# Optimization experiments

Hardware: AMD Instinct MI355X
Metric: run time of the kernel (lower is better)

## Reference

```python
import jax, jax.numpy as jnp
import numpy as np

N_NODES = 100000
EMB = 256
N_MP_EDGES = 1600000
N_SUP_EDGES = 200000


def _sage_conv(x, src, dst, W_l, b_l, W_r, n_nodes):
    # PyG SAGEConv (aggr='mean', project=False):
    #   out = lin_l(mean_{j->i} x_j) + lin_r(x_i)
    # message flows edge_index[0] (src) -> edge_index[1] (dst)
    summed = jax.ops.segment_sum(x[src], dst, num_segments=n_nodes)          # [N, d]
    cnt = jax.ops.segment_sum(jnp.ones((src.shape[0],), x.dtype), dst,
                              num_segments=n_nodes)                          # [N]
    mean = summed / jnp.maximum(cnt, 1.0)[:, None]
    return mean @ W_l.T + b_l + x @ W_r.T


def setup_inputs() -> dict:
    key = jax.random.key(0)
    ks = jax.random.split(key, 12)
    scale = 1.0 / np.sqrt(EMB)
    inp = {
        "node_embeddings": jax.random.normal(ks[0], (N_NODES, EMB), jnp.float32),
        "message_passing_edge_index": jax.random.randint(ks[1], (2, N_MP_EDGES), 0, N_NODES, jnp.int64),
        "supervision_edge_index": jax.random.randint(ks[2], (2, N_SUP_EDGES), 0, N_NODES, jnp.int64),
    }
    for i in range(3):
        inp[f"W_l{i+1}"] = jax.random.normal(ks[3 + 3 * i], (EMB, EMB), jnp.float32) * scale
        inp[f"b_l{i+1}"] = jnp.zeros((EMB,), jnp.float32)
        inp[f"W_r{i+1}"] = jax.random.normal(ks[4 + 3 * i], (EMB, EMB), jnp.float32) * scale
    return inp


def reference(node_embeddings, message_passing_edge_index, supervision_edge_index,
              W_l1, b_l1, W_r1, W_l2, b_l2, W_r2, W_l3, b_l3, W_r3):
    src = message_passing_edge_index[0]
    dst = message_passing_edge_index[1]
    n = node_embeddings.shape[0]

    x = _sage_conv(node_embeddings, src, dst, W_l1, b_l1, W_r1, n)
    x = jax.nn.relu(x)
    x = _sage_conv(x, src, dst, W_l2, b_l2, W_r2, n)
    x = jax.nn.relu(x)
    x = _sage_conv(x, src, dst, W_l3, b_l3, W_r3, n)

    s = supervision_edge_index[0]
    d = supervision_edge_index[1]
    scores = jnp.sum(x[s] * x[d], axis=1)  # [n_sup_edges]
    return scores
```

## Files before the change

kernel.cpp:

```cpp
#include <hip/hip_runtime.h>
#include <hip/hip_bf16.h>

#define N_NODES 100000
#define EMB 256
#define N_MP 1600000
#define N_SUP 200000

typedef __attribute__((ext_vector_type(4))) float f32x4;
typedef __attribute__((ext_vector_type(2))) float f32x2;
typedef __attribute__((ext_vector_type(8))) short s16x8;
typedef unsigned char uchar;

__device__ __forceinline__ int clampi(int v, int lo, int hi) {
    return v < lo ? lo : (v > hi ? hi : v);
}
__device__ __forceinline__ ushort f2bf(float f) {
    unsigned u = __float_as_uint(f);
    u += 0x7fffu + ((u >> 16) & 1u);
    return (ushort)(u >> 16);
}
__device__ __forceinline__ float bf2f(ushort h) {
    return __uint_as_float(((unsigned)h) << 16);
}
template <bool HI>
__device__ __forceinline__ f32x2 fp8_to_f32x2(unsigned w) {
    return __builtin_amdgcn_cvt_pk_f32_fp8(w, HI);
}
__device__ __forceinline__ unsigned f32x2_to_fp8(float a, float b) {
    return (unsigned)__builtin_amdgcn_cvt_pk_fp8_f32(a, b, 0, false) & 0xffffu;
}

#define GLOAD_LDS16(gsrc, ldst)                                                   \
    __builtin_amdgcn_global_load_lds(                                             \
        (const __attribute__((address_space(1))) void*)(gsrc),                    \
        (__attribute__((address_space(3))) void*)(ldst), 16, 0, 0)


__global__ void f2b8_kernel(const float* __restrict__ in, ushort* __restrict__ outb,
                            uchar* __restrict__ out8, int n8) {
    int i = blockIdx.x * 256 + threadIdx.x;
    if (i >= n8) return;
    const float4* p = (const float4*)(in + (size_t)i * 8);
    float4 a = p[0], b = p[1];
    ushort4 lo = make_ushort4(f2bf(a.x), f2bf(a.y), f2bf(a.z), f2bf(a.w));
    ushort4 hi = make_ushort4(f2bf(b.x), f2bf(b.y), f2bf(b.z), f2bf(b.w));
    ushort4* q = (ushort4*)(outb + (size_t)i * 8);
    q[0] = lo; q[1] = hi;
    uint2 f8;
    f8.x = f32x2_to_fp8(a.x, a.y) | (f32x2_to_fp8(a.z, a.w) << 16);
    f8.y = f32x2_to_fp8(b.x, b.y) | (f32x2_to_fp8(b.z, b.w) << 16);
    *(uint2*)(out8 + (size_t)i * 8) = f8;
}

struct W6 { const float* p[6]; };
__global__ void wcvt_kernel(W6 ws, ushort* __restrict__ outbase) {
    int m = blockIdx.x >> 5;
    int idx = (blockIdx.x & 31) * 256 + threadIdx.x;
    const float4* p = (const float4*)(ws.p[m] + (size_t)idx * 8);
    float4 a = p[0], b = p[1];
    ushort4 lo = make_ushort4(f2bf(a.x), f2bf(a.y), f2bf(a.z), f2bf(a.w));
    ushort4 hi = make_ushort4(f2bf(b.x), f2bf(b.y), f2bf(b.z), f2bf(b.w));
    ushort4* q = (ushort4*)(outbase + (size_t)m * EMB * EMB + (size_t)idx * 8);
    q[0] = lo; q[1] = hi;
}


#define BSH 9
#define NBUCK ((N_NODES + 511) / 512)
#define EPB_A 4096
#define SCAP 16384

__global__ void binit_kernel(int* __restrict__ gbfill) {
    int t = threadIdx.x;
    if (t < NBUCK) gbfill[t] = t * SCAP;
}

__global__ __launch_bounds__(1024) void bin_kernel(
    const int* __restrict__ src, const int* __restrict__ dst, int n,
    int* __restrict__ gbfill, unsigned* __restrict__ packed) {
    __shared__ int cnt[256];
    __shared__ int base[256];
    int tid = threadIdx.x;
    if (tid < 256) cnt[tid] = 0;
    __syncthreads();
    int e0 = blockIdx.x * EPB_A + tid;
    int bk[4], rank[4], sv[4];
    bool valid[4];
#pragma unroll
    for (int k = 0; k < 4; ++k) {
        int e = e0 + k * 1024;
        valid[k] = e < n;
        if (valid[k]) {
            int d = clampi(dst[e], 0, N_NODES - 1);
            sv[k] = clampi(src[e], 0, N_NODES - 1);
            bk[k] = d >> BSH;
            int dl = d & 511;
            sv[k] |= (dl << 20);
            rank[k] = atomicAdd(&cnt[bk[k]], 1);
        }
    }
    __syncthreads();
    if (tid < 256) {
        int c = cnt[tid];
        base[tid] = c > 0 ? atomicAdd(&gbfill[tid], c) : 0;
    }
    __syncthreads();
#pragma unroll
    for (int k = 0; k < 4; ++k) {
        if (valid[k]) {
            int pos = base[bk[k]] + rank[k];
            if (pos < (bk[k] + 1) * SCAP) packed[pos] = (unsigned)sv[k];
        }
    }
}

__global__ void bscan_kernel(const int* __restrict__ gbfill, int* __restrict__ bbase,
                             int* __restrict__ rp) {
    __shared__ int c[256];
    int t = threadIdx.x;
    c[t] = (t < NBUCK) ? (gbfill[t] - t * SCAP) : 0;
    __syncthreads();
    if (t == 0) {
        int run = 0;
        for (int i = 0; i < NBUCK; ++i) { int v = c[i]; c[i] = run; run += v; }
        rp[N_NODES] = run;
    }
    __syncthreads();
    if (t < NBUCK) bbase[t] = c[t];
}

__global__ __launch_bounds__(1024) void debin_kernel(
    const unsigned* __restrict__ packed, const int* __restrict__ gbfill,
    const int* __restrict__ bbase, int* __restrict__ srt, int* __restrict__ rp) {
    __shared__ int cnt[512];
    __shared__ int loc[512];
    __shared__ int wsum[8];
    int b = blockIdx.x;
    int tid = threadIdx.x;
    int lane = tid & 63, wv = tid >> 6;
    int node0 = b << BSH;
    int nn = N_NODES - node0; if (nn > 512) nn = 512;
    if (tid < 512) cnt[tid] = 0;
    __syncthreads();
    int pbase = b * SCAP;
    int bcnt = gbfill[b] - pbase;
    if (bcnt > SCAP) bcnt = SCAP;
    for (int e = tid; e < bcnt; e += 1024)
        atomicAdd(&cnt[packed[pbase + e] >> 20], 1);
    __syncthreads();
    int v = (tid < 512) ? cnt[tid] : 0;
    int t = v;
#pragma unroll
    for (int off = 1; off < 64; off <<= 1) {
        int u = __shfl_up(t, off, 64);
        if (lane >= off) t += u;
    }
    if (tid < 512 && lane == 63) wsum[wv] = t;
    __syncthreads();
    if (tid < 512) {
        int woff = 0;
        for (int i = 0; i < wv; ++i) woff += wsum[i];
        loc[tid] = woff + t - v;
        if (tid < nn) rp[node0 + tid] = bbase[b] + loc[tid];
    }
    __syncthreads();
    if (tid < 512) cnt[tid] = 0;
    __syncthreads();
    int sb = bbase[b];
    for (int e = tid; e < bcnt; e += 1024) {
        unsigned p = packed[pbase + e];
        int dl = p >> 20;
        int rank = atomicAdd(&cnt[dl], 1);
        srt[sb + loc[dl] + rank] = (int)(p & 0xFFFFFu);
    }
}


__global__ void agg_kernel(const uchar* __restrict__ x8, const int* __restrict__ rp,
                           const int* __restrict__ srt, ushort* __restrict__ outm) {
    int w = threadIdx.x >> 6;
    int lane = threadIdx.x & 63;
    int qw = lane >> 4;
    int sl = lane & 15;
    int node = blockIdx.x * 4 + w;
    if (node >= N_NODES) return;
    int beg = rp[node], end = rp[node + 1];
    int deg = end - beg;
    float acc[16];
#pragma unroll
    for (int i = 0; i < 16; ++i) acc[i] = 0.f;

    for (int bse = 0; bse < deg; bse += 64) {
        int rem = deg - bse;
        int cnt = rem < 64 ? rem : 64;
        int myidx = (lane < cnt) ? srt[beg + bse + lane] : 0;
        for (int j = 0; j < cnt; j += 4) {
            int e = j + qw;
            int s = __shfl(myidx, e < cnt ? e : 0, 64);
            if (e < cnt) {
                uint4 v = *(const uint4*)&x8[(unsigned)s * EMB + sl * 16];
                f32x2 p;
                p = fp8_to_f32x2<false>(v.x); acc[0] += p.x; acc[1] += p.y;
                p = fp8_to_f32x2<true >(v.x); acc[2] += p.x; acc[3] += p.y;
                p = fp8_to_f32x2<false>(v.y); acc[4] += p.x; acc[5] += p.y;
                p = fp8_to_f32x2<true >(v.y); acc[6] += p.x; acc[7] += p.y;
                p = fp8_to_f32x2<false>(v.z); acc[8] += p.x; acc[9] += p.y;
                p = fp8_to_f32x2<true >(v.z); acc[10] += p.x; acc[11] += p.y;
                p = fp8_to_f32x2<false>(v.w); acc[12] += p.x; acc[13] += p.y;
                p = fp8_to_f32x2<true >(v.w); acc[14] += p.x; acc[15] += p.y;
            }
        }
    }
#pragma unroll
    for (int i = 0; i < 16; ++i) acc[i] += __shfl_xor(acc[i], 32, 64);
#pragma unroll
    for (int i = 0; i < 16; ++i) acc[i] += __shfl_xor(acc[i], 16, 64);
    float inv = 1.0f / fmaxf((float)deg, 1.0f);
    if (qw == 0) {
        s16x8 o0, o1;
#pragma unroll
        for (int i = 0; i < 8; ++i) o0[i] = (short)f2bf(acc[i] * inv);
#pragma unroll
        for (int i = 0; i < 8; ++i) o1[i] = (short)f2bf(acc[8 + i] * inv);
        *(s16x8*)&outm[(size_t)node * EMB + sl * 16] = o0;
        *(s16x8*)&outm[(size_t)node * EMB + sl * 16 + 8] = o1;
    }
}


#define BM 128
#define BN 256
#define BKG 32
#define NSTEPS 16
#define ABSZ (BM * BKG)
#define BUFSZ (BM * BKG + BN * BKG)

__global__ __launch_bounds__(512) void gemm_kernel(
    const ushort* __restrict__ Am, const ushort* __restrict__ Ax,
    const ushort* __restrict__ Wl, const ushort* __restrict__ Wr,
    const float* __restrict__ bias, ushort* __restrict__ out,
    uchar* __restrict__ out8, int M, int do_relu) {
    __shared__ ushort smem[3 * BUFSZ];
    const int tid = threadIdx.x;
    const int lane = tid & 63;
    const int w = tid >> 6;
    const int m0 = blockIdx.x * BM;
    const int wr = w >> 2;
    const int wc = w & 3;

    f32x4 acc[4][4];
#pragma unroll
    for (int i = 0; i < 4; ++i)
#pragma unroll
        for (int j = 0; j < 4; ++j) acc[i][j] = (f32x4){0.f, 0.f, 0.f, 0.f};

    int ca = tid;
    int ra = ca >> 2;
    int cca = (ca & 3) ^ (ra & 3);
    int arow = m0 + ra; if (arow > M - 1) arow = M - 1;
    size_t srcA = (size_t)arow * EMB + cca * 8;
    int ldsoA = ca * 8;
    int cb0 = tid, cb1 = tid + 512;
    int rb0 = cb0 >> 2, rb1 = cb1 >> 2;
    size_t srcB0 = (size_t)rb0 * EMB + ((cb0 & 3) ^ (rb0 & 3)) * 8;
    size_t srcB1 = (size_t)rb1 * EMB + ((cb1 & 3) ^ (rb1 & 3)) * 8;
    int ldsoB0 = cb0 * 8, ldsoB1 = cb1 * 8;

    int raf[4], rbf[4];
#pragma unroll
    for (int mf = 0; mf < 4; ++mf) {
        int r = wr * 64 + mf * 16 + (lane & 15);
        raf[mf] = r * BKG + (((lane >> 4) ^ (r & 3)) * 8);
    }
#pragma unroll
    for (int nf = 0; nf < 4; ++nf) {
        int r = wc * 64 + nf * 16 + (lane & 15);
        rbf[nf] = r * BKG + (((lane >> 4) ^ (r & 3)) * 8);
    }

    GLOAD_LDS16(Am + srcA, smem + ldsoA);
    GLOAD_LDS16(Wl + srcB0, smem + ABSZ + ldsoB0);
    GLOAD_LDS16(Wl + srcB1, smem + ABSZ + ldsoB1);
    GLOAD_LDS16(Am + srcA + BKG, smem + BUFSZ + ldsoA);
    GLOAD_LDS16(Wl + srcB0 + BKG, smem + BUFSZ + ABSZ + ldsoB0);
    GLOAD_LDS16(Wl + srcB1 + BKG, smem + BUFSZ + ABSZ + ldsoB1);

    for (int s = 0; s < NSTEPS; ++s) {
        if (s < NSTEPS - 1) {
            asm volatile("s_waitcnt vmcnt(3)" ::: "memory");
        } else {
            asm volatile("s_waitcnt vmcnt(0)" ::: "memory");
        }
        __builtin_amdgcn_s_barrier();
        __builtin_amdgcn_sched_barrier(0);
        int nx = s + 2;
        if (nx < NSTEPS) {
            const ushort* A = (nx >= 8) ? Ax : Am;
            const ushort* W = (nx >= 8) ? Wr : Wl;
            int k0 = (nx & 7) * BKG;
            ushort* d = smem + (nx % 3) * BUFSZ;
            GLOAD_LDS16(A + srcA + k0, d + ldsoA);
            GLOAD_LDS16(W + srcB0 + k0, d + ABSZ + ldsoB0);
            GLOAD_LDS16(W + srcB1 + k0, d + ABSZ + ldsoB1);
        }
        const ushort* As = smem + (s % 3) * BUFSZ;
        const ushort* Bs = As + ABSZ;
        s16x8 af[4], bg[4];
#pragma unroll
        for (int mf = 0; mf < 4; ++mf) af[mf] = *(const s16x8*)&As[raf[mf]];
#pragma unroll
        for (int nf = 0; nf < 4; ++nf) bg[nf] = *(const s16x8*)&Bs[rbf[nf]];
#pragma unroll
        for (int mf = 0; mf < 4; ++mf)
#pragma unroll
            for (int nf = 0; nf < 4; ++nf)
                acc[mf][nf] = __builtin_amdgcn_mfma_f32_16x16x32_bf16(
                    af[mf], bg[nf], acc[mf][nf], 0, 0, 0);
    }
    __syncthreads();

    ushort* Cs = smem;
#pragma unroll
    for (int p = 0; p < 2; ++p) {
        if (wr == p) {
#pragma unroll
            for (int nf = 0; nf < 4; ++nf) {
                int col = wc * 64 + nf * 16 + (lane & 15);
                float bv = bias[col];
#pragma unroll
                for (int mf = 0; mf < 4; ++mf) {
                    int rl = mf * 16 + ((lane >> 4) << 2);
#pragma unroll
                    for (int q = 0; q < 4; ++q) {
                        float v = acc[mf][nf][q] + bv;
                        if (do_relu) v = fmaxf(v, 0.f);
                        Cs[(rl + q) * BN + col] = f2bf(v);
                    }
                }
            }
        }
        __syncthreads();
#pragma unroll
        for (int i = 0; i < 4; ++i) {
            int idx = i * 512 + tid;
            int row = m0 + p * 64 + (idx >> 5);
            if (row < M) {
                uint4 v = ((const uint4*)Cs)[idx];
                *(uint4*)&out[(size_t)row * EMB + (idx & 31) * 8] = v;
                if (out8) {
                    const ushort* pu = (const ushort*)&v;
                    unsigned lo = f32x2_to_fp8(bf2f(pu[0]), bf2f(pu[1])) |
                                  (f32x2_to_fp8(bf2f(pu[2]), bf2f(pu[3])) << 16);
                    unsigned hi = f32x2_to_fp8(bf2f(pu[4]), bf2f(pu[5])) |
                                  (f32x2_to_fp8(bf2f(pu[6]), bf2f(pu[7])) << 16);
                    *(uint2*)&out8[(size_t)row * EMB + (idx & 31) * 8] =
                        make_uint2(lo, hi);
                }
            }
        }
        __syncthreads();
    }
}


__global__ void score_kernel(const ushort* __restrict__ x, const int* __restrict__ sup,
                             float* __restrict__ out) {
    int w = threadIdx.x >> 6;
    int lane = threadIdx.x & 63;
    int half = lane >> 5;
    int sl = lane & 31;
    int e = blockIdx.x * 4 + w;
    if (e >= N_SUP) return;
    int s = clampi(sup[e], 0, N_NODES - 1);
    int d = clampi(sup[N_SUP + e], 0, N_NODES - 1);
    int row = half ? d : s;
    uint4 raw = *(const uint4*)&x[(unsigned)row * EMB + sl * 8];
    uint4 pr;
    pr.x = __shfl_xor(raw.x, 32, 64);
    pr.y = __shfl_xor(raw.y, 32, 64);
    pr.z = __shfl_xor(raw.z, 32, 64);
    pr.w = __shfl_xor(raw.w, 32, 64);
    float t = 0.f;
    unsigned a[4] = {raw.x, raw.y, raw.z, raw.w};
    unsigned b[4] = {pr.x, pr.y, pr.z, pr.w};
#pragma unroll
    for (int i = 0; i < 4; ++i) {
        t += bf2f((ushort)(a[i] & 0xffff)) * bf2f((ushort)(b[i] & 0xffff));
        t += bf2f((ushort)(a[i] >> 16)) * bf2f((ushort)(b[i] >> 16));
    }
#pragma unroll
    for (int off = 16; off > 0; off >>= 1) t += __shfl_xor(t, off, 64);
    if (lane == 0) out[e] = t;
}


extern "C" void kernel_launch(void* const* d_in, const int* in_sizes, int n_in,
                              void* d_out, int out_size, void* d_ws, size_t ws_size,
                              hipStream_t stream) {
    const float* x0  = (const float*)d_in[0];
    const int*   mp  = (const int*)d_in[1];
    const int*   sup = (const int*)d_in[2];
    W6 wsrc;
    wsrc.p[0] = (const float*)d_in[3];
    wsrc.p[1] = (const float*)d_in[5];
    wsrc.p[2] = (const float*)d_in[6];
    wsrc.p[3] = (const float*)d_in[8];
    wsrc.p[4] = (const float*)d_in[9];
    wsrc.p[5] = (const float*)d_in[11];
    const float* bl1 = (const float*)d_in[4];
    const float* bl2 = (const float*)d_in[7];
    const float* bl3 = (const float*)d_in[10];
    float* scores = (float*)d_out;

    const int* mp_src = mp;
    const int* mp_dst = mp + N_MP;

    char* base = (char*)d_ws;
    size_t off = 0;
    auto alloc = [&](size_t bytes) {
        void* p = base + off;
        off = (off + bytes + 255) & ~(size_t)255;
        return p;
    };
    int* rp     = (int*)alloc((N_NODES + 1) * sizeof(int));
    int* gbfill = (int*)alloc(256 * sizeof(int));
    int* bbase  = (int*)alloc(256 * sizeof(int));
    int* srt    = (int*)alloc(N_MP * sizeof(int));
    unsigned* packed = (unsigned*)alloc((size_t)NBUCK * SCAP * sizeof(unsigned));
    ushort* x0b  = (ushort*)alloc((size_t)N_NODES * EMB * sizeof(ushort));
    ushort* bufA = (ushort*)alloc((size_t)N_NODES * EMB * sizeof(ushort));
    ushort* bufB = (ushort*)alloc((size_t)N_NODES * EMB * sizeof(ushort));
    ushort* bufC = (ushort*)alloc((size_t)N_NODES * EMB * sizeof(ushort));
    uchar*  x0f8 = (uchar*)alloc((size_t)N_NODES * EMB);
    uchar*  a8   = (uchar*)alloc((size_t)N_NODES * EMB);
    ushort* Wb   = (ushort*)alloc((size_t)6 * EMB * EMB * sizeof(ushort));
    (void)ws_size; (void)n_in; (void)in_sizes; (void)out_size;

    f2b8_kernel<<<(N_NODES * EMB / 8 + 255) / 256, 256, 0, stream>>>(
        x0, x0b, x0f8, N_NODES * EMB / 8);
    wcvt_kernel<<<192, 256, 0, stream>>>(wsrc, Wb);

    binit_kernel<<<1, 256, 0, stream>>>(gbfill);
    bin_kernel<<<(N_MP + EPB_A - 1) / EPB_A, 1024, 0, stream>>>(
        mp_src, mp_dst, N_MP, gbfill, packed);
    bscan_kernel<<<1, 256, 0, stream>>>(gbfill, bbase, rp);
    debin_kernel<<<NBUCK, 1024, 0, stream>>>(packed, gbfill, bbase, srt, rp);

    dim3 gemm_grid((N_NODES + BM - 1) / BM, 1);
    int agg_blocks = (N_NODES + 3) / 4;

    ushort* Wl1 = Wb + 0 * EMB * EMB; ushort* Wr1 = Wb + 1 * EMB * EMB;
    ushort* Wl2 = Wb + 2 * EMB * EMB; ushort* Wr2 = Wb + 3 * EMB * EMB;
    ushort* Wl3 = Wb + 4 * EMB * EMB; ushort* Wr3 = Wb + 5 * EMB * EMB;

    agg_kernel<<<agg_blocks, 256, 0, stream>>>(x0f8, rp, srt, bufC);
    gemm_kernel<<<gemm_grid, 512, 0, stream>>>(bufC, x0b, Wl1, Wr1, bl1, bufA, a8, N_NODES, 1);

    agg_kernel<<<agg_blocks, 256, 0, stream>>>(a8, rp, srt, bufC);
    gemm_kernel<<<gemm_grid, 512, 0, stream>>>(bufC, bufA, Wl2, Wr2, bl2, bufB, a8, N_NODES, 1);

    agg_kernel<<<agg_blocks, 256, 0, stream>>>(a8, rp, srt, bufC);
    gemm_kernel<<<gemm_grid, 512, 0, stream>>>(bufC, bufB, Wl3, Wr3, bl3, bufA,
                                               (uchar*)nullptr, N_NODES, 0);

    score_kernel<<<(N_SUP + 3) / 4, 256, 0, stream>>>(bufA, sup, scores);
}
```

Before: 434.7 us.

## Store aggregated means in fp8 and run the lin_l GEMM half with fp8 MFMA

```diff
diff --git a/kernel.cpp b/kernel.cpp
--- a/kernel.cpp
+++ b/kernel.cpp
@@ -53,15 +53,21 @@
 }
 
 struct W6 { const float* p[6]; };
-__global__ void wcvt_kernel(W6 ws, ushort* __restrict__ outbase) {
+__global__ void wcvt_kernel(W6 ws, ushort* __restrict__ outb, uchar* __restrict__ out8) {
     int m = blockIdx.x >> 5;
     int idx = (blockIdx.x & 31) * 256 + threadIdx.x;
     const float4* p = (const float4*)(ws.p[m] + (size_t)idx * 8);
     float4 a = p[0], b = p[1];
     ushort4 lo = make_ushort4(f2bf(a.x), f2bf(a.y), f2bf(a.z), f2bf(a.w));
     ushort4 hi = make_ushort4(f2bf(b.x), f2bf(b.y), f2bf(b.z), f2bf(b.w));
-    ushort4* q = (ushort4*)(outbase + (size_t)m * EMB * EMB + (size_t)idx * 8);
+    ushort4* q = (ushort4*)(outb + (size_t)m * EMB * EMB + (size_t)idx * 8);
     q[0] = lo; q[1] = hi;
+    if (!(m & 1)) {
+        uint2 f8;
+        f8.x = f32x2_to_fp8(a.x, a.y) | (f32x2_to_fp8(a.z, a.w) << 16);
+        f8.y = f32x2_to_fp8(b.x, b.y) | (f32x2_to_fp8(b.z, b.w) << 16);
+        *(uint2*)(out8 + (size_t)(m >> 1) * EMB * EMB + (size_t)idx * 8) = f8;
+    }
 }
 
 
@@ -177,7 +183,7 @@
 
 
 __global__ void agg_kernel(const uchar* __restrict__ x8, const int* __restrict__ rp,
-                           const int* __restrict__ srt, ushort* __restrict__ outm) {
+                           const int* __restrict__ srt, uchar* __restrict__ outm8) {
     int w = threadIdx.x >> 6;
     int lane = threadIdx.x & 63;
     int qw = lane >> 4;
@@ -217,27 +223,29 @@
     for (int i = 0; i < 16; ++i) acc[i] += __shfl_xor(acc[i], 16, 64);
     float inv = 1.0f / fmaxf((float)deg, 1.0f);
     if (qw == 0) {
-        s16x8 o0, o1;
-#pragma unroll
-        for (int i = 0; i < 8; ++i) o0[i] = (short)f2bf(acc[i] * inv);
-#pragma unroll
-        for (int i = 0; i < 8; ++i) o1[i] = (short)f2bf(acc[8 + i] * inv);
-        *(s16x8*)&outm[(size_t)node * EMB + sl * 16] = o0;
-        *(s16x8*)&outm[(size_t)node * EMB + sl * 16 + 8] = o1;
+        uint4 o;
+        o.x = f32x2_to_fp8(acc[0] * inv, acc[1] * inv) |
+              (f32x2_to_fp8(acc[2] * inv, acc[3] * inv) << 16);
+        o.y = f32x2_to_fp8(acc[4] * inv, acc[5] * inv) |
+              (f32x2_to_fp8(acc[6] * inv, acc[7] * inv) << 16);
+        o.z = f32x2_to_fp8(acc[8] * inv, acc[9] * inv) |
+              (f32x2_to_fp8(acc[10] * inv, acc[11] * inv) << 16);
+        o.w = f32x2_to_fp8(acc[12] * inv, acc[13] * inv) |
+              (f32x2_to_fp8(acc[14] * inv, acc[15] * inv) << 16);
+        *(uint4*)&outm8[(size_t)node * EMB + sl * 16] = o;
     }
 }
 
 
 #define BM 128
 #define BN 256
-#define BKG 32
-#define NSTEPS 16
-#define ABSZ (BM * BKG)
-#define BUFSZ (BM * BKG + BN * BKG)
+#define NSTEPS 12
+#define BUFSZ 12288
+#define AREG 8192
 
 __global__ __launch_bounds__(512) void gemm_kernel(
-    const ushort* __restrict__ Am, const ushort* __restrict__ Ax,
-    const ushort* __restrict__ Wl, const ushort* __restrict__ Wr,
+    const uchar* __restrict__ Am8, const ushort* __restrict__ Ax,
+    const uchar* __restrict__ Wl8, const ushort* __restrict__ Wr,
     const float* __restrict__ bias, ushort* __restrict__ out,
     uchar* __restrict__ out8, int M, int do_relu) {
     __shared__ ushort smem[3 * BUFSZ];
@@ -247,6 +255,7 @@
     const int m0 = blockIdx.x * BM;
     const int wr = w >> 2;
     const int wc = w & 3;
+    const int g = lane >> 4;
 
     f32x4 acc[4][4];
 #pragma unroll
@@ -254,36 +263,54 @@
 #pragma unroll
         for (int j = 0; j < 4; ++j) acc[i][j] = (f32x4){0.f, 0.f, 0.f, 0.f};
 
-    int ca = tid;
-    int ra = ca >> 2;
-    int cca = (ca & 3) ^ (ra & 3);
-    int arow = m0 + ra; if (arow > M - 1) arow = M - 1;
-    size_t srcA = (size_t)arow * EMB + cca * 8;
-    int ldsoA = ca * 8;
-    int cb0 = tid, cb1 = tid + 512;
-    int rb0 = cb0 >> 2, rb1 = cb1 >> 2;
-    size_t srcB0 = (size_t)rb0 * EMB + ((cb0 & 3) ^ (rb0 & 3)) * 8;
-    size_t srcB1 = (size_t)rb1 * EMB + ((cb1 & 3) ^ (rb1 & 3)) * 8;
-    int ldsoB0 = cb0 * 8, ldsoB1 = cb1 * 8;
-
-    int raf[4], rbf[4];
+    int cA = tid;
+    int rA = cA >> 2, qA = (cA & 3) ^ (rA & 3);
+    int arow = m0 + rA; if (arow > M - 1) arow = M - 1;
+    int cB0 = tid, cB1 = tid + 512;
+    int rB0 = cB0 >> 2, qB0 = (cB0 & 3) ^ (rB0 & 3);
+    int rB1 = cB1 >> 2, qB1 = (cB1 & 3) ^ (rB1 & 3);
+    size_t srcA8 = (size_t)arow * 256 + qA * 16;
+    size_t srcB08 = (size_t)rB0 * 256 + qB0 * 16;
+    size_t srcB18 = (size_t)rB1 * 256 + qB1 * 16;
+    size_t srcAb = (size_t)arow * EMB + qA * 8;
+    size_t srcB0b = (size_t)rB0 * EMB + qB0 * 8;
+    size_t srcB1b = (size_t)rB1 * EMB + qB1 * 8;
+    int ldsoA = cA * 16;
+    int ldsoB0 = AREG + cB0 * 16;
+    int ldsoB1 = AREG + cB1 * 16;
+
+    int raf8[4][2], rbf8[4][2], rafb[4], rbfb[4];
 #pragma unroll
     for (int mf = 0; mf < 4; ++mf) {
         int r = wr * 64 + mf * 16 + (lane & 15);
-        raf[mf] = r * BKG + (((lane >> 4) ^ (r & 3)) * 8);
+        rafb[mf] = r * 64 + (((g) ^ (r & 3)) << 4);
+#pragma unroll
+        for (int ks = 0; ks < 2; ++ks) {
+            int hi = ks * 2 + (g >> 1);
+            raf8[mf][ks] = r * 64 + ((hi ^ (r & 3)) << 4) + ((g & 1) * 8);
+        }
     }
 #pragma unroll
     for (int nf = 0; nf < 4; ++nf) {
         int r = wc * 64 + nf * 16 + (lane & 15);
-        rbf[nf] = r * BKG + (((lane >> 4) ^ (r & 3)) * 8);
-    }
-
-    GLOAD_LDS16(Am + srcA, smem + ldsoA);
-    GLOAD_LDS16(Wl + srcB0, smem + ABSZ + ldsoB0);
-    GLOAD_LDS16(Wl + srcB1, smem + ABSZ + ldsoB1);
-    GLOAD_LDS16(Am + srcA + BKG, smem + BUFSZ + ldsoA);
-    GLOAD_LDS16(Wl + srcB0 + BKG, smem + BUFSZ + ABSZ + ldsoB0);
-    GLOAD_LDS16(Wl + srcB1 + BKG, smem + BUFSZ + ABSZ + ldsoB1);
+        rbfb[nf] = r * 64 + (((g) ^ (r & 3)) << 4);
+#pragma unroll
+        for (int ks = 0; ks < 2; ++ks) {
+            int hi = ks * 2 + (g >> 1);
+            rbf8[nf][ks] = r * 64 + ((hi ^ (r & 3)) << 4) + ((g & 1) * 8);
+        }
+    }
+
+    {
+        uchar* d0 = (uchar*)smem;
+        uchar* d1 = (uchar*)smem + BUFSZ * 2;
+        GLOAD_LDS16(Am8 + srcA8 + 0, d0 + ldsoA);
+        GLOAD_LDS16(Wl8 + srcB08 + 0, d0 + ldsoB0);
+        GLOAD_LDS16(Wl8 + srcB18 + 0, d0 + ldsoB1);
+        GLOAD_LDS16(Am8 + srcA8 + 64, d1 + ldsoA);
+        GLOAD_LDS16(Wl8 + srcB08 + 64, d1 + ldsoB0);
+        GLOAD_LDS16(Wl8 + srcB18 + 64, d1 + ldsoB1);
+    }
 
     for (int s = 0; s < NSTEPS; ++s) {
         if (s < NSTEPS - 1) {
@@ -295,27 +322,55 @@
         __builtin_amdgcn_sched_barrier(0);
         int nx = s + 2;
         if (nx < NSTEPS) {
-            const ushort* A = (nx >= 8) ? Ax : Am;
-            const ushort* W = (nx >= 8) ? Wr : Wl;
-            int k0 = (nx & 7) * BKG;
-            ushort* d = smem + (nx % 3) * BUFSZ;
-            GLOAD_LDS16(A + srcA + k0, d + ldsoA);
-            GLOAD_LDS16(W + srcB0 + k0, d + ABSZ + ldsoB0);
-            GLOAD_LDS16(W + srcB1 + k0, d + ABSZ + ldsoB1);
-        }
-        const ushort* As = smem + (s % 3) * BUFSZ;
-        const ushort* Bs = As + ABSZ;
-        s16x8 af[4], bg[4];
-#pragma unroll
-        for (int mf = 0; mf < 4; ++mf) af[mf] = *(const s16x8*)&As[raf[mf]];
-#pragma unroll
-        for (int nf = 0; nf < 4; ++nf) bg[nf] = *(const s16x8*)&Bs[rbf[nf]];
-#pragma unroll
-        for (int mf = 0; mf < 4; ++mf)
-#pragma unroll
-            for (int nf = 0; nf < 4; ++nf)
-                acc[mf][nf] = __builtin_amdgcn_mfma_f32_16x16x32_bf16(
-                    af[mf], bg[nf], acc[mf][nf], 0, 0, 0);
+            uchar* d = (uchar*)smem + (nx % 3) * BUFSZ * 2;
+            if (nx < 4) {
+                int k0 = nx * 64;
+                GLOAD_LDS16(Am8 + srcA8 + k0, d + ldsoA);
+                GLOAD_LDS16(Wl8 + srcB08 + k0, d + ldsoB0);
+                GLOAD_LDS16(Wl8 + srcB18 + k0, d + ldsoB1);
+            } else {
+                int k0 = (nx - 4) * 32;
+                GLOAD_LDS16(Ax + srcAb + k0, d + ldsoA);
+                GLOAD_LDS16(Wr + srcB0b + k0, d + ldsoB0);
+                GLOAD_LDS16(Wr + srcB1b + k0, d + ldsoB1);
+            }
+        }
+        const char* Asb = (const char*)smem + (s % 3) * BUFSZ * 2;
+        const char* Bsb = Asb + AREG;
+        if (s < 4) {
+            long af[4][2], bg[4][2];
+#pragma unroll
+            for (int mf = 0; mf < 4; ++mf) {
+                af[mf][0] = *(const long*)(Asb + raf8[mf][0]);
+                af[mf][1] = *(const long*)(Asb + raf8[mf][1]);
+            }
+#pragma unroll
+            for (int nf = 0; nf < 4; ++nf) {
+                bg[nf][0] = *(const long*)(Bsb + rbf8[nf][0]);
+                bg[nf][1] = *(const long*)(Bsb + rbf8[nf][1]);
+            }
+#pragma unroll
+            for (int mf = 0; mf < 4; ++mf)
+#pragma unroll
+                for (int nf = 0; nf < 4; ++nf) {
+                    acc[mf][nf] = __builtin_amdgcn_mfma_f32_16x16x32_fp8_fp8(
+                        af[mf][0], bg[nf][0], acc[mf][nf], 0, 0, 0);
+                    acc[mf][nf] = __builtin_amdgcn_mfma_f32_16x16x32_fp8_fp8(
+                        af[mf][1], bg[nf][1], acc[mf][nf], 0, 0, 0);
+                }
+        } else {
+            s16x8 af[4], bg[4];
+#pragma unroll
+            for (int mf = 0; mf < 4; ++mf) af[mf] = *(const s16x8*)(Asb + rafb[mf]);
+#pragma unroll
+            for (int nf = 0; nf < 4; ++nf) bg[nf] = *(const s16x8*)(Bsb + rbfb[nf]);
+#pragma unroll
+            for (int mf = 0; mf < 4; ++mf)
+#pragma unroll
+                for (int nf = 0; nf < 4; ++nf)
+                    acc[mf][nf] = __builtin_amdgcn_mfma_f32_16x16x32_bf16(
+                        af[mf], bg[nf], acc[mf][nf], 0, 0, 0);
+        }
     }
     __syncthreads();
 
@@ -430,15 +485,16 @@
     ushort* x0b  = (ushort*)alloc((size_t)N_NODES * EMB * sizeof(ushort));
     ushort* bufA = (ushort*)alloc((size_t)N_NODES * EMB * sizeof(ushort));
     ushort* bufB = (ushort*)alloc((size_t)N_NODES * EMB * sizeof(ushort));
-    ushort* bufC = (ushort*)alloc((size_t)N_NODES * EMB * sizeof(ushort));
+    uchar*  bufC8 = (uchar*)alloc((size_t)N_NODES * EMB);
     uchar*  x0f8 = (uchar*)alloc((size_t)N_NODES * EMB);
     uchar*  a8   = (uchar*)alloc((size_t)N_NODES * EMB);
     ushort* Wb   = (ushort*)alloc((size_t)6 * EMB * EMB * sizeof(ushort));
+    uchar*  W8   = (uchar*)alloc((size_t)3 * EMB * EMB);
     (void)ws_size; (void)n_in; (void)in_sizes; (void)out_size;
 
     f2b8_kernel<<<(N_NODES * EMB / 8 + 255) / 256, 256, 0, stream>>>(
         x0, x0b, x0f8, N_NODES * EMB / 8);
-    wcvt_kernel<<<192, 256, 0, stream>>>(wsrc, Wb);
+    wcvt_kernel<<<192, 256, 0, stream>>>(wsrc, Wb, W8);
 
     binit_kernel<<<1, 256, 0, stream>>>(gbfill);
     bin_kernel<<<(N_MP + EPB_A - 1) / EPB_A, 1024, 0, stream>>>(
@@ -449,18 +505,21 @@
     dim3 gemm_grid((N_NODES + BM - 1) / BM, 1);
     int agg_blocks = (N_NODES + 3) / 4;
 
-    ushort* Wl1 = Wb + 0 * EMB * EMB; ushort* Wr1 = Wb + 1 * EMB * EMB;
-    ushort* Wl2 = Wb + 2 * EMB * EMB; ushort* Wr2 = Wb + 3 * EMB * EMB;
-    ushort* Wl3 = Wb + 4 * EMB * EMB; ushort* Wr3 = Wb + 5 * EMB * EMB;
-
-    agg_kernel<<<agg_blocks, 256, 0, stream>>>(x0f8, rp, srt, bufC);
-    gemm_kernel<<<gemm_grid, 512, 0, stream>>>(bufC, x0b, Wl1, Wr1, bl1, bufA, a8, N_NODES, 1);
-
-    agg_kernel<<<agg_blocks, 256, 0, stream>>>(a8, rp, srt, bufC);
-    gemm_kernel<<<gemm_grid, 512, 0, stream>>>(bufC, bufA, Wl2, Wr2, bl2, bufB, a8, N_NODES, 1);
-
-    agg_kernel<<<agg_blocks, 256, 0, stream>>>(a8, rp, srt, bufC);
-    gemm_kernel<<<gemm_grid, 512, 0, stream>>>(bufC, bufB, Wl3, Wr3, bl3, bufA,
+    ushort* Wr1 = Wb + 1 * EMB * EMB;
+    ushort* Wr2 = Wb + 3 * EMB * EMB;
+    ushort* Wr3 = Wb + 5 * EMB * EMB;
+    uchar* Wl1_8 = W8 + 0 * EMB * EMB;
+    uchar* Wl2_8 = W8 + 1 * EMB * EMB;
+    uchar* Wl3_8 = W8 + 2 * EMB * EMB;
+
+    agg_kernel<<<agg_blocks, 256, 0, stream>>>(x0f8, rp, srt, bufC8);
+    gemm_kernel<<<gemm_grid, 512, 0, stream>>>(bufC8, x0b, Wl1_8, Wr1, bl1, bufA, a8, N_NODES, 1);
+
+    agg_kernel<<<agg_blocks, 256, 0, stream>>>(a8, rp, srt, bufC8);
+    gemm_kernel<<<gemm_grid, 512, 0, stream>>>(bufC8, bufA, Wl2_8, Wr2, bl2, bufB, a8, N_NODES, 1);
+
+    agg_kernel<<<agg_blocks, 256, 0, stream>>>(a8, rp, srt, bufC8);
+    gemm_kernel<<<gemm_grid, 512, 0, stream>>>(bufC8, bufB, Wl3_8, Wr3, bl3, bufA,
                                                (uchar*)nullptr, N_NODES, 0);
 
     score_kernel<<<(N_SUP + 3) / 4, 256, 0, stream>>>(bufA, sup, scores);
```

After: 412.1 us. -5.2%, faster.
